# Optimization experiments

Measured on AMD Instinct MI355X. Metric: run time of the kernel, lower is better.

## Reference

```python
import jax, jax.numpy as jnp
import numpy as np

KW = 3          # kernel_width
PAD = (KW - 1) // 2


def setup_inputs() -> dict:
    key = jax.random.key(0)
    ks = jax.random.split(key, 7)
    B, Lq, Lk, D, C = 8, 1024, 1024, 512, 512  # D=q_size, C=k_size
    return {
        "q": jax.random.normal(ks[0], (B, Lq, D), jnp.float32),
        "k": jax.random.normal(ks[1], (B, Lk, C), jnp.float32),
        "W_kernel": jax.random.normal(ks[2], (D, C * KW), jnp.float32) * (1.0 / np.sqrt(D)),
        "b_kernel": jax.random.normal(ks[3], (C * KW,), jnp.float32) * 0.02,
        "W_bias": jax.random.normal(ks[4], (D, 1), jnp.float32) * (1.0 / np.sqrt(D)),
        "b_bias": jax.random.normal(ks[5], (1,), jnp.float32) * 0.02,
        "bias_b": jax.random.normal(ks[6], (1,), jnp.float32),
    }


def reference(q, k, W_kernel, b_kernel, W_bias, b_bias, bias_b):
    B, Lq, D = q.shape
    _, Lk, C = k.shape
    # per-(batch, query) dynamic conv kernels: [B, Lq, C, KW]
    kernel = (q @ W_kernel + b_kernel).reshape(B, Lq, C, KW)
    # per-(batch, query) scalar bias: [B, Lq]
    bias = (q @ W_bias + b_bias)[..., 0]
    # windowed view of k (cross-correlation with 'same' padding)
    kpad = jnp.pad(k, ((0, 0), (PAD, PAD), (0, 0)))  # [B, Lk+2*PAD, C]
    win_idx = jnp.arange(Lk)[:, None] + jnp.arange(KW)[None, :]  # [Lk, KW]
    kwin = kpad[:, win_idx, :]  # [B, Lk, KW, C]
    # a[b,i,j] = sum_{c,w} kernel[b,i,c,w] * kpad[b, j+w, c] + bias[b,i] + bias_b
    a_ij = jnp.einsum('bicw,bjwc->bij', kernel, kwin)
    return a_ij + bias[:, :, None] + bias_b
```

## Files before the change

### kernel.cpp

```cpp
#include <hip/hip_runtime.h>


typedef __attribute__((ext_vector_type(8))) short s8vec;
typedef __attribute__((ext_vector_type(4))) float floatx4;

__device__ __forceinline__ unsigned short f2bf(float f) {
    union { float f; unsigned u; } v; v.f = f;
    unsigned r = (v.u + 0x7FFFu + ((v.u >> 16) & 1u)) >> 16;
    return (unsigned short)r;
}

__device__ __forceinline__ void gl2lds16(const void* g, void* l) {
    __builtin_amdgcn_global_load_lds(
        (__attribute__((address_space(1))) void*)(g),
        (__attribute__((address_space(3))) void*)(l), 16, 0, 0);
}

__global__ void cvt_all(const float* __restrict__ q, const float* __restrict__ k,
                        unsigned short* __restrict__ qbf, unsigned short* __restrict__ kp,
                        const float* __restrict__ Wb, const float* __restrict__ b_bias,
                        float* __restrict__ biasb) {
    int blk = blockIdx.x;
    if (blk < 4104) {
        int t = blk * 256 + threadIdx.x;
        if (t < 524288) {
            const float4* p = (const float4*)q + 2 * (size_t)t;
            float4 a = p[0], b = p[1];
            union { unsigned short s[8]; uint4 v; } o;
            o.s[0]=f2bf(a.x); o.s[1]=f2bf(a.y); o.s[2]=f2bf(a.z); o.s[3]=f2bf(a.w);
            o.s[4]=f2bf(b.x); o.s[5]=f2bf(b.y); o.s[6]=f2bf(b.z); o.s[7]=f2bf(b.w);
            ((uint4*)qbf)[t] = o.v;
        } else if (t < 1048576) {
            int e8 = t - 524288;
            size_t e = (size_t)e8 * 8;
            int b = e8 >> 16;
            int j = (e8 >> 6) & 1023;
            int c = (e8 & 63) * 8;
            const float4* p = (const float4*)(k + e);
            float4 a = p[0], bb = p[1];
            union { unsigned short s[8]; uint4 v; } o;
            o.s[0]=f2bf(a.x); o.s[1]=f2bf(a.y); o.s[2]=f2bf(a.z); o.s[3]=f2bf(a.w);
            o.s[4]=f2bf(bb.x); o.s[5]=f2bf(bb.y); o.s[6]=f2bf(bb.z); o.s[7]=f2bf(bb.w);
            *(uint4*)(kp + ((size_t)(b * 1028 + j + 1) * 512 + c)) = o.v;
        } else if (t < 1050624) {
            int z = t - 1048576;
            int b = z >> 8, r = (z >> 6) & 3, ch = z & 63;
            int row = r ? (1024 + r) : 0;
            *(uint4*)(kp + ((size_t)(b * 1028 + row) * 512 + ch * 8)) = make_uint4(0u,0u,0u,0u);
        }
    } else {
        int row  = (blk - 4104) * 4 + (threadIdx.x >> 6);
        int lane = threadIdx.x & 63;
        const float4* qr = (const float4*)(q + (size_t)row * 512) + lane * 2;
        const float4* wb = (const float4*)Wb + lane * 2;
        float4 a0 = qr[0], a1 = qr[1], b0 = wb[0], b1 = wb[1];
        float s = a0.x*b0.x + a0.y*b0.y + a0.z*b0.z + a0.w*b0.w
                + a1.x*b1.x + a1.y*b1.y + a1.z*b1.z + a1.w*b1.w;
        #pragma unroll
        for (int off = 32; off > 0; off >>= 1) s += __shfl_down(s, off);
        if (lane == 0) biasb[row] = s + b_bias[0];
    }
}

__global__ void prep_Wt(const float* __restrict__ W, unsigned short* __restrict__ Wt) {
    __shared__ float lds[32][33];
    int cw0 = blockIdx.x * 32, d0 = blockIdx.y * 32;
    int tx = threadIdx.x, ty = threadIdx.y;
    lds[ty][tx] = W[(size_t)(d0 + ty) * 1536 + cw0 + tx];
    __syncthreads();
    int cw = cw0 + ty;
    int c = cw / 3, w = cw % 3;
    Wt[((size_t)(w * 512 + c)) * 512 + d0 + tx] = f2bf(lds[tx][ty]);
}

__global__ __launch_bounds__(128) void gemm_A(const unsigned short* __restrict__ Abf,
                                              const unsigned short* __restrict__ Bbf,
                                              const float* __restrict__ b_kernel,
                                              unsigned short* __restrict__ G) {
    __shared__ unsigned short lds_a[64 * 32];
    __shared__ unsigned short lds_b[128 * 32];
    int g = blockIdx.x;
    int xcd = g & 7, slot = g >> 3;
    int i_blk = xcd * 16 + (slot & 15);
    int n_blk = slot >> 4;
    int i0 = i_blk * 64, n0 = n_blk * 128;
    int tid = threadIdx.x, wid = tid >> 6, lane = tid & 63;
    floatx4 acc[4][4] = {};

    for (int kk = 0; kk < 512; kk += 32) {
        #pragma unroll
        for (int s = 0; s < 6; ++s) {
            int t = s * 2 + wid;
            if (t < 4) {
                const unsigned short* ga = Abf + (size_t)(i0 + t * 16 + (lane >> 2)) * 512 + kk + (lane & 3) * 8;
                gl2lds16(ga, (char*)lds_a + t * 1024);
            } else {
                int u = t - 4;
                const unsigned short* gb = Bbf + (size_t)(n0 + u * 16 + (lane >> 2)) * 512 + kk + (lane & 3) * 8;
                gl2lds16(gb, (char*)lds_b + u * 1024);
            }
        }
        __syncthreads();
        int ra = lane & 15, q8 = (lane >> 4) * 8;
        s8vec af[4], bf_[4];
        #pragma unroll
        for (int mi = 0; mi < 4; mi++)
            af[mi] = *(const s8vec*)(lds_a + (mi * 16 + ra) * 32 + q8);
        #pragma unroll
        for (int ni = 0; ni < 4; ni++)
            bf_[ni] = *(const s8vec*)(lds_b + (wid * 64 + ni * 16 + ra) * 32 + q8);
        #pragma unroll
        for (int mi = 0; mi < 4; mi++)
            #pragma unroll
            for (int ni = 0; ni < 4; ni++)
                acc[mi][ni] = __builtin_amdgcn_mfma_f32_16x16x32_bf16(af[mi], bf_[ni], acc[mi][ni], 0, 0, 0);
        __syncthreads();
    }

    int cl = lane & 15, qd = lane >> 4;
    #pragma unroll
    for (int mi = 0; mi < 4; mi++) {
        #pragma unroll
        for (int ni = 0; ni < 4; ni++) {
            int n_all = n0 + wid * 64 + ni * 16 + cl;
            int c = n_all & 511, w = n_all >> 9;
            float bk = b_kernel[c * 3 + w];
            #pragma unroll
            for (int r = 0; r < 4; r++) {
                int i_g = i0 + mi * 16 + qd * 4 + r;
                int b = i_g >> 10, ii = i_g & 1023;
                G[((size_t)((b * 3 + w) * 1024 + ii)) * 512 + c] = f2bf(acc[mi][ni][r] + bk);
            }
        }
    }
}

__global__ __launch_bounds__(128) void gemm_B(const unsigned short* __restrict__ G,
                                              const unsigned short* __restrict__ kp,
                                              const float* __restrict__ biasb,
                                              const float* __restrict__ bias_b,
                                              float* __restrict__ out) {
    __shared__ unsigned short lds_a[3 * 64 * 32];
    __shared__ unsigned short lds_k[144 * 32];
    int g = blockIdx.x;
    int b = g & 7, slot = g >> 3;
    int j0 = (slot & 7) * 128;
    int i0 = (slot >> 3) * 64;
    int tid = threadIdx.x, wid = tid >> 6, lane = tid & 63;
    floatx4 acc[4][4] = {};
    const unsigned short* Gb  = G  + (size_t)b * 3 * 1024 * 512;
    const unsigned short* kpb = kp + (size_t)b * 1028 * 512;
    float bb = bias_b[0];

    for (int kk = 0; kk < 512; kk += 32) {
        #pragma unroll
        for (int s = 0; s < 11; ++s) {
            int t = s * 2 + wid;
            if (t < 21) {
                if (t < 12) {
                    int w = t >> 2, chunk = t & 3;
                    const unsigned short* ga = Gb + (size_t)(w * 1024 + i0 + chunk * 16 + (lane >> 2)) * 512
                                                  + kk + (lane & 3) * 8;
                    gl2lds16(ga, (char*)lds_a + t * 1024);
                } else {
                    int u = t - 12;
                    const unsigned short* gk = kpb + (size_t)(j0 + u * 16 + (lane >> 2)) * 512
                                                   + kk + (lane & 3) * 8;
                    gl2lds16(gk, (char*)lds_k + u * 1024);
                }
            }
        }
        __syncthreads();
        int ra = lane & 15, q8 = (lane >> 4) * 8;
        #pragma unroll
        for (int w = 0; w < 3; ++w) {
            s8vec af[4], bfr[4];
            #pragma unroll
            for (int mi = 0; mi < 4; mi++)
                af[mi] = *(const s8vec*)(lds_a + (w * 64 + mi * 16 + ra) * 32 + q8);
            #pragma unroll
            for (int ni = 0; ni < 4; ni++) {
                int rr = wid * 64 + ni * 16 + ra + w;
                bfr[ni] = *(const s8vec*)(lds_k + rr * 32 + q8);
            }
            #pragma unroll
            for (int mi = 0; mi < 4; mi++)
                #pragma unroll
                for (int ni = 0; ni < 4; ni++)
                    acc[mi][ni] = __builtin_amdgcn_mfma_f32_16x16x32_bf16(af[mi], bfr[ni], acc[mi][ni], 0, 0, 0);
        }
        __syncthreads();
    }

    int cl = lane & 15, qd = lane >> 4;
    #pragma unroll
    for (int mi = 0; mi < 4; mi++) {
        #pragma unroll
        for (int r = 0; r < 4; r++) {
            int i_loc = mi * 16 + qd * 4 + r;
            float bv = biasb[b * 1024 + i0 + i_loc] + bb;
            #pragma unroll
            for (int ni = 0; ni < 4; ni++) {
                int j_loc = wid * 64 + ni * 16 + cl;
                out[((size_t)(b * 1024 + i0 + i_loc)) * 1024 + j0 + j_loc] = acc[mi][ni][r] + bv;
            }
        }
    }
}

extern "C" void kernel_launch(void* const* d_in, const int* in_sizes, int n_in,
                              void* d_out, int out_size, void* d_ws, size_t ws_size,
                              hipStream_t stream) {
    const float* q        = (const float*)d_in[0];
    const float* k        = (const float*)d_in[1];
    const float* W_kernel = (const float*)d_in[2];
    const float* b_kernel = (const float*)d_in[3];
    const float* W_bias   = (const float*)d_in[4];
    const float* b_bias   = (const float*)d_in[5];
    const float* bias_b   = (const float*)d_in[6];
    float* out = (float*)d_out;

    char* ws = (char*)d_ws;
    unsigned short* q_bf = (unsigned short*)(ws);
    unsigned short* kp   = (unsigned short*)(ws + 8388608);
    unsigned short* Wt   = (unsigned short*)(ws + 8388608 + 8421376 + 16384);
    unsigned short* G    = (unsigned short*)(ws + 8388608 + 8421376 + 16384 + 1572864);
    float*          bsb  = (float*)(ws + 8388608 + 8421376 + 16384 + 1572864 + 25165824);

    cvt_all<<<6152, 256, 0, stream>>>(q, k, q_bf, kp, W_bias, b_bias, bsb);
    prep_Wt<<<dim3(48, 16), dim3(32, 32), 0, stream>>>(W_kernel, Wt);
    gemm_A<<<1536, 128, 0, stream>>>(q_bf, Wt, b_kernel, G);
    gemm_B<<<1024, 128, 0, stream>>>(G, kp, bsb, bias_b, out);
}
```

Baseline: 152.0 us.

## Fuse weight transpose into conversion kernel and double gemm_A K-step to 64

```diff
diff --git a/kernel.cpp b/kernel.cpp
--- a/kernel.cpp
+++ b/kernel.cpp
@@ -19,7 +19,8 @@
 __global__ void cvt_all(const float* __restrict__ q, const float* __restrict__ k,
                         unsigned short* __restrict__ qbf, unsigned short* __restrict__ kp,
                         const float* __restrict__ Wb, const float* __restrict__ b_bias,
-                        float* __restrict__ biasb) {
+                        float* __restrict__ biasb,
+                        const float* __restrict__ W, unsigned short* __restrict__ Wt) {
     int blk = blockIdx.x;
     if (blk < 4104) {
         int t = blk * 256 + threadIdx.x;
@@ -48,7 +49,7 @@
             int row = r ? (1024 + r) : 0;
             *(uint4*)(kp + ((size_t)(b * 1028 + row) * 512 + ch * 8)) = make_uint4(0u,0u,0u,0u);
         }
-    } else {
+    } else if (blk < 6152) {
         int row  = (blk - 4104) * 4 + (threadIdx.x >> 6);
         int lane = threadIdx.x & 63;
         const float4* qr = (const float4*)(q + (size_t)row * 512) + lane * 2;
@@ -59,26 +60,32 @@
         #pragma unroll
         for (int off = 32; off > 0; off >>= 1) s += __shfl_down(s, off);
         if (lane == 0) biasb[row] = s + b_bias[0];
-    }
-}
-
-__global__ void prep_Wt(const float* __restrict__ W, unsigned short* __restrict__ Wt) {
-    __shared__ float lds[32][33];
-    int cw0 = blockIdx.x * 32, d0 = blockIdx.y * 32;
-    int tx = threadIdx.x, ty = threadIdx.y;
-    lds[ty][tx] = W[(size_t)(d0 + ty) * 1536 + cw0 + tx];
-    __syncthreads();
-    int cw = cw0 + ty;
-    int c = cw / 3, w = cw % 3;
-    Wt[((size_t)(w * 512 + c)) * 512 + d0 + tx] = f2bf(lds[tx][ty]);
+    } else {
+        __shared__ float lds[32][33];
+        int p = blk - 6152;
+        int cw0 = (p % 48) * 32, d0 = (p / 48) * 32;
+        int tid = threadIdx.x;
+        #pragma unroll
+        for (int rep = 0; rep < 4; rep++) {
+            int e = rep * 256 + tid, dy = e >> 5, dx = e & 31;
+            lds[dy][dx] = W[(size_t)(d0 + dy) * 1536 + cw0 + dx];
+        }
+        __syncthreads();
+        #pragma unroll
+        for (int rep = 0; rep < 4; rep++) {
+            int e = rep * 256 + tid, cy = e >> 5, cx = e & 31;
+            int cw = cw0 + cy, c = cw / 3, w = cw % 3;
+            Wt[((size_t)(w * 512 + c)) * 512 + d0 + cx] = f2bf(lds[cx][cy]);
+        }
+    }
 }
 
 __global__ __launch_bounds__(128) void gemm_A(const unsigned short* __restrict__ Abf,
                                               const unsigned short* __restrict__ Bbf,
                                               const float* __restrict__ b_kernel,
                                               unsigned short* __restrict__ G) {
-    __shared__ unsigned short lds_a[64 * 32];
-    __shared__ unsigned short lds_b[128 * 32];
+    __shared__ unsigned short lds_a[64 * 64];
+    __shared__ unsigned short lds_b[128 * 64];
     int g = blockIdx.x;
     int xcd = g & 7, slot = g >> 3;
     int i_blk = xcd * 16 + (slot & 15);
@@ -87,33 +94,36 @@
     int tid = threadIdx.x, wid = tid >> 6, lane = tid & 63;
     floatx4 acc[4][4] = {};
 
-    for (int kk = 0; kk < 512; kk += 32) {
-        #pragma unroll
-        for (int s = 0; s < 6; ++s) {
+    for (int kk = 0; kk < 512; kk += 64) {
+        #pragma unroll
+        for (int s = 0; s < 12; ++s) {
             int t = s * 2 + wid;
-            if (t < 4) {
-                const unsigned short* ga = Abf + (size_t)(i0 + t * 16 + (lane >> 2)) * 512 + kk + (lane & 3) * 8;
+            if (t < 8) {
+                const unsigned short* ga = Abf + (size_t)(i0 + t * 8 + (lane >> 3)) * 512 + kk + (lane & 7) * 8;
                 gl2lds16(ga, (char*)lds_a + t * 1024);
             } else {
-                int u = t - 4;
-                const unsigned short* gb = Bbf + (size_t)(n0 + u * 16 + (lane >> 2)) * 512 + kk + (lane & 3) * 8;
+                int u = t - 8;
+                const unsigned short* gb = Bbf + (size_t)(n0 + u * 8 + (lane >> 3)) * 512 + kk + (lane & 7) * 8;
                 gl2lds16(gb, (char*)lds_b + u * 1024);
             }
         }
         __syncthreads();
         int ra = lane & 15, q8 = (lane >> 4) * 8;
-        s8vec af[4], bf_[4];
-        #pragma unroll
-        for (int mi = 0; mi < 4; mi++)
-            af[mi] = *(const s8vec*)(lds_a + (mi * 16 + ra) * 32 + q8);
-        #pragma unroll
-        for (int ni = 0; ni < 4; ni++)
-            bf_[ni] = *(const s8vec*)(lds_b + (wid * 64 + ni * 16 + ra) * 32 + q8);
-        #pragma unroll
-        for (int mi = 0; mi < 4; mi++)
+        #pragma unroll
+        for (int h = 0; h < 2; ++h) {
+            s8vec af[4], bf_[4];
+            #pragma unroll
+            for (int mi = 0; mi < 4; mi++)
+                af[mi] = *(const s8vec*)(lds_a + (mi * 16 + ra) * 64 + h * 32 + q8);
             #pragma unroll
             for (int ni = 0; ni < 4; ni++)
-                acc[mi][ni] = __builtin_amdgcn_mfma_f32_16x16x32_bf16(af[mi], bf_[ni], acc[mi][ni], 0, 0, 0);
+                bf_[ni] = *(const s8vec*)(lds_b + (wid * 64 + ni * 16 + ra) * 64 + h * 32 + q8);
+            #pragma unroll
+            for (int mi = 0; mi < 4; mi++)
+                #pragma unroll
+                for (int ni = 0; ni < 4; ni++)
+                    acc[mi][ni] = __builtin_amdgcn_mfma_f32_16x16x32_bf16(af[mi], bf_[ni], acc[mi][ni], 0, 0, 0);
+        }
         __syncthreads();
     }
 
@@ -227,8 +237,7 @@
     unsigned short* G    = (unsigned short*)(ws + 8388608 + 8421376 + 16384 + 1572864);
     float*          bsb  = (float*)(ws + 8388608 + 8421376 + 16384 + 1572864 + 25165824);
 
-    cvt_all<<<6152, 256, 0, stream>>>(q, k, q_bf, kp, W_bias, b_bias, bsb);
-    prep_Wt<<<dim3(48, 16), dim3(32, 32), 0, stream>>>(W_kernel, Wt);
+    cvt_all<<<6920, 256, 0, stream>>>(q, k, q_bf, kp, W_bias, b_bias, bsb, W_kernel, Wt);
     gemm_A<<<1536, 128, 0, stream>>>(q_bf, Wt, b_kernel, G);
     gemm_B<<<1024, 128, 0, stream>>>(G, kp, bsb, bias_b, out);
 }
```

Measured after the change: 152.9 us. No clear change (+0.6%).
